# Kernel tuning notes

Hardware: AMD Instinct MI355X
Metric: run time of the kernel (lower is better)

## Reference

```python
import jax, jax.numpy as jnp
import numpy as np

S, D, H, L, FF = 4096, 128, 4, 3, 1024
DH = D // H
LN_EPS = 1e-5


def _layernorm(x, g, b):
    m = jnp.mean(x, axis=-1, keepdims=True)
    v = jnp.mean((x - m) ** 2, axis=-1, keepdims=True)
    return (x - m) * jax.lax.rsqrt(v + LN_EPS) * g + b


def setup_inputs() -> dict:
    key = jax.random.key(0)
    ks = jax.random.split(key, 16)
    w = lambda k, shp, s=0.05: jax.random.normal(k, shp, dtype=jnp.float32) * s
    return {
        "src": jax.random.normal(ks[0], (S, 1, D), dtype=jnp.float32),
        # per-layer transformer params, stacked on leading L axis
        "Wqkv": w(ks[1], (L, 3 * D, D)),
        "bqkv": jnp.zeros((L, 3 * D), jnp.float32),
        "Wo": w(ks[2], (L, D, D)),
        "bo": jnp.zeros((L, D), jnp.float32),
        "ln1_g": jnp.ones((L, D), jnp.float32),
        "ln1_b": jnp.zeros((L, D), jnp.float32),
        "W1": w(ks[3], (L, FF, D)),
        "b1": jnp.zeros((L, FF), jnp.float32),
        "W2": w(ks[4], (L, D, FF)),
        "b2": jnp.zeros((L, D), jnp.float32),
        "ln2_g": jnp.ones((L, D), jnp.float32),
        "ln2_b": jnp.zeros((L, D), jnp.float32),
        "fc1_W": w(ks[5], (D, D)),
        "fc1_b": jnp.zeros((D,), jnp.float32),
        "fc2_W": w(ks[6], (D, D)),
        "fc2_b": jnp.zeros((D,), jnp.float32),
    }


def reference(src, Wqkv, bqkv, Wo, bo, ln1_g, ln1_b, W1, b1, W2, b2,
              ln2_g, ln2_b, fc1_W, fc1_b, fc2_W, fc2_b):
    x = src[:, 0, :]  # [S, D] (batch=1, squeezed as in the torch module)
    scale = 1.0 / np.sqrt(DH).astype(np.float32)
    for l in range(L):  # small fixed layer count
        # --- self-attention (post-norm, as in torch TransformerEncoderLayer, eval mode) ---
        qkv = x @ Wqkv[l].T + bqkv[l]                      # [S, 3D]
        q, k, v = jnp.split(qkv, 3, axis=-1)
        q = q.reshape(S, H, DH)
        k = k.reshape(S, H, DH)
        v = v.reshape(S, H, DH)
        att = jax.nn.softmax(jnp.einsum('shd,thd->hst', q, k) * scale, axis=-1)
        o = jnp.einsum('hst,thd->shd', att, v).reshape(S, D)
        o = o @ Wo[l].T + bo[l]
        x = _layernorm(x + o, ln1_g[l], ln1_b[l])
        # --- feed-forward ---
        f = jax.nn.relu(x @ W1[l].T + b1[l]) @ W2[l].T + b2[l]
        x = _layernorm(x + f, ln2_g[l], ln2_b[l])
    # head
    x = jax.nn.relu(x @ fc1_W.T + fc1_b)
    x = x @ fc2_W.T + fc2_b
    # pairwise cosine similarity, clamped at min 1e-6 (vectorized form of pCosineSim)
    xn = x / jnp.linalg.norm(x, axis=1, keepdims=True)
    return jnp.maximum(xn @ xn.T, 1e-6)
```

## Files before the change

kernel.cpp:

```cpp
#include <hip/hip_runtime.h>
#include <math.h>

#define S 4096
#define QK_SCALE 0.17677669529663687f
#define LOG2E    1.44269504088896f
#define SPLIT 8
#define KS (S / SPLIT)

typedef _Float16 f16x8 __attribute__((ext_vector_type(8)));
typedef _Float16 f16x4 __attribute__((ext_vector_type(4)));
typedef _Float16 f16x2 __attribute__((ext_vector_type(2)));
typedef float f32x4 __attribute__((ext_vector_type(4)));

template<int R>
__device__ __forceinline__ void stageT(_Float16 (*dst)[136], const _Float16* __restrict__ src,
                                       int ld, int row0, int col0, int tid) {
    int r = tid >> 4, cb = (tid & 15) * 8;
#pragma unroll
    for (int v = 0; v < R / 16; v++)
        *(f16x8*)&dst[v * 16 + r][cb] =
            *(const f16x8*)(src + (size_t)(row0 + v * 16 + r) * ld + col0 + cb);
}

__global__ __launch_bounds__(256) void setup_cvt(const float* __restrict__ q,
                                                 const float* __restrict__ wo,
                                                 const float* __restrict__ w1,
                                                 const float* __restrict__ w2,
                                                 const float* __restrict__ f1,
                                                 const float* __restrict__ f2,
                                                 _Float16* __restrict__ dst,
                                                 const float* __restrict__ a,
                                                 float* __restrict__ x,
                                                 _Float16* __restrict__ xh)
{
    int bb = blockIdx.x;
    if (bb < 992) {
        const float* src; size_t dof; int lb;
        if (bb < 144)      { src = q;  dof = 0;      lb = bb; }
        else if (bb < 192) { src = wo; dof = 147456; lb = bb - 144; }
        else if (bb < 576) { src = w1; dof = 196608; lb = bb - 192; }
        else if (bb < 960) { src = w2; dof = 589824; lb = bb - 576; }
        else if (bb < 976) { src = f1; dof = 983040; lb = bb - 960; }
        else               { src = f2; dof = 999424; lb = bb - 976; }
        int i = lb * 1024 + threadIdx.x * 4;
        float4 v = *(const float4*)(src + i);
        f16x4 h = {(_Float16)v.x, (_Float16)v.y, (_Float16)v.z, (_Float16)v.w};
        *(f16x4*)(dst + dof + i) = h;
    } else {
        int i = (bb - 992) * 256 + threadIdx.x;
        float4 v = ((const float4*)a)[i];
        ((float4*)x)[i] = v;
        f16x4 h = {(_Float16)v.x, (_Float16)v.y, (_Float16)v.z, (_Float16)v.w};
        ((f16x4*)xh)[i] = h;
    }
}

__global__ __launch_bounds__(256) void gemm_qkv(const _Float16* __restrict__ xh,
                                                const _Float16* __restrict__ Wh,
                                                const float* __restrict__ bias,
                                                _Float16* __restrict__ qh,
                                                _Float16* __restrict__ kh,
                                                _Float16* __restrict__ vt)
{
    __shared__ _Float16 Ah[16][136], Bh[128][136];
    int tid = threadIdx.x, w = tid >> 6, l = tid & 63, lc = l & 15, lr = l >> 4;
    int m0 = blockIdx.x * 16, by = blockIdx.y;

    stageT<16>(Ah, xh, 128, m0, 0, tid);
    stageT<128>(Bh, Wh, 128, by * 128, 0, tid);
    __syncthreads();

    f32x4 acc[2];
#pragma unroll
    for (int j = 0; j < 2; j++) acc[j] = {0.f, 0.f, 0.f, 0.f};
#pragma unroll
    for (int ks = 0; ks < 4; ks++) {
        f16x8 af = *(const f16x8*)&Ah[lc][ks * 32 + lr * 8];
#pragma unroll
        for (int j = 0; j < 2; j++) {
            f16x8 bf = *(const f16x8*)&Bh[w * 32 + j * 16 + lc][ks * 32 + lr * 8];
            acc[j] = __builtin_amdgcn_mfma_f32_16x16x32_f16(af, bf, acc[j], 0, 0, 0);
        }
    }

    int mb = m0 + lr * 4;
#pragma unroll
    for (int j = 0; j < 2; j++) {
        int n = w * 32 + j * 16 + lc;
        float bb = bias[by * 128 + n];
        if (by == 0) {
#pragma unroll
            for (int r = 0; r < 4; r++)
                qh[(size_t)(mb + r) * 128 + n] =
                    (_Float16)((acc[j][r] + bb) * (QK_SCALE * LOG2E));
        } else if (by == 1) {
            int hh = n >> 5, d = n & 31;
#pragma unroll
            for (int r = 0; r < 4; r++)
                kh[((size_t)hh * S + mb + r) * 32 + d] = (_Float16)(acc[j][r] + bb);
        } else {
            f16x4 pk;
#pragma unroll
            for (int r = 0; r < 4; r++) pk[r] = (_Float16)(acc[j][r] + bb);
            *(f16x4*)&vt[(size_t)n * S + mb] = pk;
        }
    }
}

__global__ __launch_bounds__(256) void attn_mfma(const _Float16* __restrict__ qh,
                                                 const _Float16* __restrict__ kh,
                                                 const _Float16* __restrict__ vt,
                                                 _Float16* __restrict__ part,
                                                 float* __restrict__ mll)
{
    __shared__ _Float16 Ks[2][64][32];
    __shared__ _Float16 Vt[2][32][72];
    __shared__ _Float16 Ps[4][16][72];
    int h = blockIdx.y, q0 = blockIdx.x * 64, z = blockIdx.z;
    int tid = threadIdx.x;
    int w = tid >> 6, l = tid & 63;
    int lc = l & 15, lr = l >> 4;

    f16x8 qf = *(const f16x8*)&qh[(size_t)(q0 + w * 16 + lc) * 128 + h * 32 + lr * 8];

    const _Float16* khh = kh + (size_t)h * S * 32;
    const _Float16* vth = vt + (size_t)h * 32 * S;

    int krow = tid >> 2, kcol = (tid & 3) * 8;
    int vrow = tid >> 3, vcol = (tid & 7) * 8;

    f32x4 o0 = {0.f, 0.f, 0.f, 0.f}, o1 = {0.f, 0.f, 0.f, 0.f};
    float lp = 0.f;

    int k0 = z * KS;
    {
        f16x8 kr = *(const f16x8*)&khh[(size_t)(k0 + krow) * 32 + kcol];
        f16x8 vr = *(const f16x8*)&vth[(size_t)vrow * S + k0 + vcol];
        *(f16x8*)&Ks[0][krow][kcol] = kr;
        *(f16x8*)&Vt[0][vrow][vcol] = vr;
    }
    __syncthreads();

    int cur = 0;
#pragma unroll 1
    for (int t8 = 0; t8 < KS / 64; t8++) {
        bool more = (t8 + 1 < KS / 64);
        f16x8 kr, vr;
        if (more) {
            int kn = k0 + (t8 + 1) * 64;
            kr = *(const f16x8*)&khh[(size_t)(kn + krow) * 32 + kcol];
            vr = *(const f16x8*)&vth[(size_t)vrow * S + kn + vcol];
        }

        f32x4 st[4];
#pragma unroll
        for (int t = 0; t < 4; t++) {
            f16x8 kf = *(const f16x8*)&Ks[cur][t * 16 + lc][lr * 8];
            f32x4 zz = {0.f, 0.f, 0.f, 0.f};
            st[t] = __builtin_amdgcn_mfma_f32_16x16x32_f16(kf, qf, zz, 0, 0, 0);
        }
#pragma unroll
        for (int t = 0; t < 4; t++) {
            float p0 = exp2f(st[t][0]), p1 = exp2f(st[t][1]);
            float p2 = exp2f(st[t][2]), p3 = exp2f(st[t][3]);
            lp += (p0 + p1) + (p2 + p3);
            f16x2 h0 = {(_Float16)p0, (_Float16)p1};
            f16x2 h1 = {(_Float16)p2, (_Float16)p3};
            *(f16x2*)&Ps[w][lc][t * 16 + lr * 4]     = h0;
            *(f16x2*)&Ps[w][lc][t * 16 + lr * 4 + 2] = h1;
        }
        asm volatile("s_waitcnt lgkmcnt(0)" ::: "memory");
#pragma unroll
        for (int ch = 0; ch < 2; ch++) {
            f16x8 pf = *(const f16x8*)&Ps[w][lc][ch * 32 + lr * 8];
            f16x8 v0 = *(const f16x8*)&Vt[cur][lc][ch * 32 + lr * 8];
            f16x8 v1 = *(const f16x8*)&Vt[cur][16 + lc][ch * 32 + lr * 8];
            o0 = __builtin_amdgcn_mfma_f32_16x16x32_f16(pf, v0, o0, 0, 0, 0);
            o1 = __builtin_amdgcn_mfma_f32_16x16x32_f16(pf, v1, o1, 0, 0, 0);
        }
        if (more) {
            *(f16x8*)&Ks[cur ^ 1][krow][kcol] = kr;
            *(f16x8*)&Vt[cur ^ 1][vrow][vcol] = vr;
            __syncthreads();
        }
        cur ^= 1;
    }

    lp += __shfl_xor(lp, 16);
    lp += __shfl_xor(lp, 32);

    _Float16* pz = part + (size_t)z * 524288;
#pragma unroll
    for (int i = 0; i < 4; i++) {
        int q = q0 + w * 16 + lr * 4 + i;
        pz[(size_t)q * 128 + h * 32 + lc]      = (_Float16)o0[i];
        pz[(size_t)q * 128 + h * 32 + 16 + lc] = (_Float16)o1[i];
    }
    if (l < 16) mll[((size_t)z * 4 + h) * 4096 + q0 + w * 16 + lc] = lp;
}

__global__ __launch_bounds__(256) void wo_ln_merge(const _Float16* __restrict__ part,
                                                   const float* __restrict__ mll,
                                                   const _Float16* __restrict__ Wh,
                                                   const float* __restrict__ bias,
                                                   float* __restrict__ x,
                                                   _Float16* __restrict__ xh,
                                                   const float* __restrict__ g,
                                                   const float* __restrict__ b)
{
    __shared__ _Float16 Ah[16][136], Bh[128][136];
    __shared__ float Red[16][4][2];
    int tid = threadIdx.x, w = tid >> 6, l = tid & 63, lc = l & 15, lr = l >> 4;
    int m0 = blockIdx.x * 16;

    {
        int row = tid >> 4, col0 = (tid & 15) * 8;
        int q = m0 + row, hh = col0 >> 5;
        float lsum = 0.f;
#pragma unroll
        for (int s = 0; s < SPLIT; s++) lsum += mll[((size_t)s * 4 + hh) * 4096 + q];
        float am[8];
#pragma unroll
        for (int e = 0; e < 8; e++) am[e] = 0.f;
#pragma unroll
        for (int s = 0; s < SPLIT; s++) {
            f16x8 t = *(const f16x8*)&part[(size_t)s * 524288 + (size_t)q * 128 + col0];
#pragma unroll
            for (int e = 0; e < 8; e++) am[e] += (float)t[e];
        }
        float inv = 1.f / lsum;
        f16x8 hv;
#pragma unroll
        for (int e = 0; e < 8; e++) hv[e] = (_Float16)(am[e] * inv);
        *(f16x8*)&Ah[row][col0] = hv;
    }
    stageT<128>(Bh, Wh, 128, 0, 0, tid);
    __syncthreads();

    f32x4 acc[2];
#pragma unroll
    for (int j = 0; j < 2; j++) acc[j] = {0.f, 0.f, 0.f, 0.f};
#pragma unroll
    for (int ks = 0; ks < 4; ks++) {
        f16x8 af = *(const f16x8*)&Ah[lc][ks * 32 + lr * 8];
#pragma unroll
        for (int j = 0; j < 2; j++) {
            f16x8 bf = *(const f16x8*)&Bh[w * 32 + j * 16 + lc][ks * 32 + lr * 8];
            acc[j] = __builtin_amdgcn_mfma_f32_16x16x32_f16(af, bf, acc[j], 0, 0, 0);
        }
    }

#pragma unroll
    for (int j = 0; j < 2; j++) {
        int n = w * 32 + j * 16 + lc;
        float bb = bias[n];
#pragma unroll
        for (int r = 0; r < 4; r++)
            acc[j][r] += bb + x[(size_t)(m0 + lr * 4 + r) * 128 + n];
    }
#pragma unroll
    for (int r = 0; r < 4; r++) {
        float s1 = acc[0][r] + acc[1][r];
        float s2 = acc[0][r] * acc[0][r] + acc[1][r] * acc[1][r];
#pragma unroll
        for (int off = 1; off < 16; off <<= 1) {
            s1 += __shfl_xor(s1, off);
            s2 += __shfl_xor(s2, off);
        }
        if (lc == 0) { Red[lr * 4 + r][w][0] = s1; Red[lr * 4 + r][w][1] = s2; }
    }
    __syncthreads();
#pragma unroll
    for (int r = 0; r < 4; r++) {
        int rl = lr * 4 + r;
        float S1 = (Red[rl][0][0] + Red[rl][1][0]) + (Red[rl][2][0] + Red[rl][3][0]);
        float S2 = (Red[rl][0][1] + Red[rl][1][1]) + (Red[rl][2][1] + Red[rl][3][1]);
        float mean = S1 * (1.0f / 128.0f);
        float var = S2 * (1.0f / 128.0f) - mean * mean;
        float inv = rsqrtf(var + 1e-5f);
        int m = m0 + rl;
#pragma unroll
        for (int j = 0; j < 2; j++) {
            int n = w * 32 + j * 16 + lc;
            float o = (acc[j][r] - mean) * inv * g[n] + b[n];
            x[(size_t)m * 128 + n] = o;
            xh[(size_t)m * 128 + n] = (_Float16)o;
        }
    }
}

__global__ __launch_bounds__(256) void ffn_pair(const _Float16* __restrict__ xh,
                                                const _Float16* __restrict__ W1h,
                                                const float* __restrict__ b1,
                                                const _Float16* __restrict__ W2h,
                                                _Float16* __restrict__ wpart)
{
    __shared__ _Float16 Ah[64][136], Bh[128][136];
    int tid = threadIdx.x, w = tid >> 6, l = tid & 63, lc = l & 15, lr = l >> 4;
    int wr = w >> 1, wc = w & 1;
    int m0 = blockIdx.x * 64, c = blockIdx.y;

    stageT<64>(Ah, xh, 128, m0, 0, tid);
    stageT<128>(Bh, W1h, 128, c * 128, 0, tid);
    __syncthreads();

    f32x4 acc[2][4];
#pragma unroll
    for (int i = 0; i < 2; i++)
#pragma unroll
        for (int j = 0; j < 4; j++) acc[i][j] = {0.f, 0.f, 0.f, 0.f};
#pragma unroll
    for (int ks = 0; ks < 4; ks++) {
        f16x8 af0 = *(const f16x8*)&Ah[wr * 32 + lc][ks * 32 + lr * 8];
        f16x8 af1 = *(const f16x8*)&Ah[wr * 32 + 16 + lc][ks * 32 + lr * 8];
#pragma unroll
        for (int j = 0; j < 4; j++) {
            f16x8 bf = *(const f16x8*)&Bh[wc * 64 + j * 16 + lc][ks * 32 + lr * 8];
            acc[0][j] = __builtin_amdgcn_mfma_f32_16x16x32_f16(af0, bf, acc[0][j], 0, 0, 0);
            acc[1][j] = __builtin_amdgcn_mfma_f32_16x16x32_f16(af1, bf, acc[1][j], 0, 0, 0);
        }
    }
    __syncthreads();

#pragma unroll
    for (int i = 0; i < 2; i++)
#pragma unroll
        for (int j = 0; j < 4; j++) {
            int n = wc * 64 + j * 16 + lc;
            float bb = b1[c * 128 + n];
#pragma unroll
            for (int r = 0; r < 4; r++)
                Ah[wr * 32 + i * 16 + lr * 4 + r][n] =
                    (_Float16)fmaxf(acc[i][j][r] + bb, 0.f);
        }
    stageT<128>(Bh, W2h, 1024, 0, c * 128, tid);
    __syncthreads();

    f32x4 oacc[2][4];
#pragma unroll
    for (int i = 0; i < 2; i++)
#pragma unroll
        for (int j = 0; j < 4; j++) oacc[i][j] = {0.f, 0.f, 0.f, 0.f};
#pragma unroll
    for (int ks = 0; ks < 4; ks++) {
        f16x8 af0 = *(const f16x8*)&Ah[wr * 32 + lc][ks * 32 + lr * 8];
        f16x8 af1 = *(const f16x8*)&Ah[wr * 32 + 16 + lc][ks * 32 + lr * 8];
#pragma unroll
        for (int j = 0; j < 4; j++) {
            f16x8 bf = *(const f16x8*)&Bh[wc * 64 + j * 16 + lc][ks * 32 + lr * 8];
            oacc[0][j] = __builtin_amdgcn_mfma_f32_16x16x32_f16(af0, bf, oacc[0][j], 0, 0, 0);
            oacc[1][j] = __builtin_amdgcn_mfma_f32_16x16x32_f16(af1, bf, oacc[1][j], 0, 0, 0);
        }
    }

    _Float16* pz = wpart + (size_t)c * 524288;
#pragma unroll
    for (int i = 0; i < 2; i++) {
        int mb = m0 + wr * 32 + i * 16 + lr * 4;
#pragma unroll
        for (int j = 0; j < 4; j++) {
            int n = wc * 64 + j * 16 + lc;
#pragma unroll
            for (int r = 0; r < 4; r++)
                pz[(size_t)(mb + r) * 128 + n] = (_Float16)oacc[i][j][r];
        }
    }
}

__global__ __launch_bounds__(256) void reduce8_ln(const _Float16* __restrict__ part,
                                                  const float* __restrict__ bias,
                                                  float* __restrict__ x,
                                                  _Float16* __restrict__ xh,
                                                  const float* __restrict__ g,
                                                  const float* __restrict__ b)
{
    int row  = blockIdx.x * 4 + (threadIdx.x >> 6);
    int lane = threadIdx.x & 63;
    size_t base = (size_t)row * 128;
    int c = lane * 2;
    float a0 = 0.f, a1 = 0.f;
#pragma unroll
    for (int s = 0; s < 8; s++) {
        f16x2 p = *(const f16x2*)&part[(size_t)s * 524288 + base + c];
        a0 += (float)p[0]; a1 += (float)p[1];
    }
    float2 bv = *(const float2*)&bias[c];
    float2 xv = *(const float2*)&x[base + c];
    a0 += bv.x + xv.x; a1 += bv.y + xv.y;
    float s = a0 + a1;
#pragma unroll
    for (int off = 32; off; off >>= 1) s += __shfl_xor(s, off);
    float mean = s * (1.0f / 128.0f);
    float d0 = a0 - mean, d1 = a1 - mean;
    float v = d0 * d0 + d1 * d1;
#pragma unroll
    for (int off = 32; off; off >>= 1) v += __shfl_xor(v, off);
    float inv = rsqrtf(v * (1.0f / 128.0f) + 1e-5f);
    float2 gv = *(const float2*)&g[c];
    float2 bb = *(const float2*)&b[c];
    float o0 = d0 * inv * gv.x + bb.x, o1 = d1 * inv * gv.y + bb.y;
    float2 r; r.x = o0; r.y = o1;
    *(float2*)&x[base + c] = r;
    f16x2 rh = {(_Float16)o0, (_Float16)o1};
    *(f16x2*)&xh[base + c] = rh;
}

__global__ __launch_bounds__(256) void fc_fused(const _Float16* __restrict__ xh,
                                                const _Float16* __restrict__ W1h,
                                                const float* __restrict__ b1f,
                                                const _Float16* __restrict__ W2h,
                                                const float* __restrict__ b2f,
                                                _Float16* __restrict__ aoh)
{
    __shared__ _Float16 Ah[16][136], Bh[128][136];
    __shared__ float Red[16][4];
    int tid = threadIdx.x, w = tid >> 6, l = tid & 63, lc = l & 15, lr = l >> 4;
    int m0 = blockIdx.x * 16;

    stageT<16>(Ah, xh, 128, m0, 0, tid);
    stageT<128>(Bh, W1h, 128, 0, 0, tid);
    __syncthreads();

    f32x4 acc[2];
#pragma unroll
    for (int j = 0; j < 2; j++) acc[j] = {0.f, 0.f, 0.f, 0.f};
#pragma unroll
    for (int ks = 0; ks < 4; ks++) {
        f16x8 af = *(const f16x8*)&Ah[lc][ks * 32 + lr * 8];
#pragma unroll
        for (int j = 0; j < 2; j++) {
            f16x8 bf = *(const f16x8*)&Bh[w * 32 + j * 16 + lc][ks * 32 + lr * 8];
            acc[j] = __builtin_amdgcn_mfma_f32_16x16x32_f16(af, bf, acc[j], 0, 0, 0);
        }
    }
    __syncthreads();
#pragma unroll
    for (int j = 0; j < 2; j++) {
        int n = w * 32 + j * 16 + lc;
        float bb = b1f[n];
#pragma unroll
        for (int r = 0; r < 4; r++)
            Ah[lr * 4 + r][n] = (_Float16)fmaxf(acc[j][r] + bb, 0.f);
    }
    stageT<128>(Bh, W2h, 128, 0, 0, tid);
    __syncthreads();

    f32x4 o[2];
#pragma unroll
    for (int j = 0; j < 2; j++) o[j] = {0.f, 0.f, 0.f, 0.f};
#pragma unroll
    for (int ks = 0; ks < 4; ks++) {
        f16x8 af = *(const f16x8*)&Ah[lc][ks * 32 + lr * 8];
#pragma unroll
        for (int j = 0; j < 2; j++) {
            f16x8 bf = *(const f16x8*)&Bh[w * 32 + j * 16 + lc][ks * 32 + lr * 8];
            o[j] = __builtin_amdgcn_mfma_f32_16x16x32_f16(af, bf, o[j], 0, 0, 0);
        }
    }
#pragma unroll
    for (int j = 0; j < 2; j++) {
        float bb = b2f[w * 32 + j * 16 + lc];
#pragma unroll
        for (int r = 0; r < 4; r++) o[j][r] += bb;
    }
#pragma unroll
    for (int r = 0; r < 4; r++) {
        float s2 = o[0][r] * o[0][r] + o[1][r] * o[1][r];
#pragma unroll
        for (int off = 1; off < 16; off <<= 1) s2 += __shfl_xor(s2, off);
        if (lc == 0) Red[lr * 4 + r][w] = s2;
    }
    __syncthreads();
#pragma unroll
    for (int r = 0; r < 4; r++) {
        int rl = lr * 4 + r;
        float inv = rsqrtf((Red[rl][0] + Red[rl][1]) + (Red[rl][2] + Red[rl][3]));
        int m = m0 + rl;
#pragma unroll
        for (int j = 0; j < 2; j++) {
            int n = w * 32 + j * 16 + lc;
            aoh[(size_t)m * 128 + n] = (_Float16)(o[j][r] * inv);
        }
    }
}

__global__ __launch_bounds__(256) void gram_f16(const _Float16* __restrict__ aoh,
                                                float* __restrict__ C)
{
    __shared__ _Float16 Ah[64][136], Bh[128][136];
    int tid = threadIdx.x, w = tid >> 6, l = tid & 63, lc = l & 15, lr = l >> 4;
    int wr = w >> 1, wc = w & 1;
    int m0 = blockIdx.x * 64, n0 = blockIdx.y * 128;

    stageT<64>(Ah, aoh, 128, m0, 0, tid);
    stageT<128>(Bh, aoh, 128, n0, 0, tid);
    __syncthreads();

    f32x4 acc[2][4];
#pragma unroll
    for (int i = 0; i < 2; i++)
#pragma unroll
        for (int j = 0; j < 4; j++) acc[i][j] = {0.f, 0.f, 0.f, 0.f};
#pragma unroll
    for (int ks = 0; ks < 4; ks++) {
        f16x8 af0 = *(const f16x8*)&Ah[wr * 32 + lc][ks * 32 + lr * 8];
        f16x8 af1 = *(const f16x8*)&Ah[wr * 32 + 16 + lc][ks * 32 + lr * 8];
#pragma unroll
        for (int j = 0; j < 4; j++) {
            f16x8 bf = *(const f16x8*)&Bh[wc * 64 + j * 16 + lc][ks * 32 + lr * 8];
            acc[0][j] = __builtin_amdgcn_mfma_f32_16x16x32_f16(af0, bf, acc[0][j], 0, 0, 0);
            acc[1][j] = __builtin_amdgcn_mfma_f32_16x16x32_f16(af1, bf, acc[1][j], 0, 0, 0);
        }
    }

#pragma unroll
    for (int i = 0; i < 2; i++) {
        int mb = m0 + wr * 32 + i * 16 + lr * 4;
#pragma unroll
        for (int j = 0; j < 4; j++) {
            int n = n0 + wc * 64 + j * 16 + lc;
#pragma unroll
            for (int r = 0; r < 4; r++)
                C[(size_t)(mb + r) * 4096 + n] = fmaxf(acc[i][j][r], 1e-6f);
        }
    }
}

extern "C" void kernel_launch(void* const* d_in, const int* in_sizes, int n_in,
                              void* d_out, int out_size, void* d_ws, size_t ws_size,
                              hipStream_t stream)
{
    const float* src  = (const float*)d_in[0];
    const float* Wqkv = (const float*)d_in[1];
    const float* bqkv = (const float*)d_in[2];
    const float* Wo   = (const float*)d_in[3];
    const float* bo   = (const float*)d_in[4];
    const float* ln1g = (const float*)d_in[5];
    const float* ln1b = (const float*)d_in[6];
    const float* W1   = (const float*)d_in[7];
    const float* b1   = (const float*)d_in[8];
    const float* W2   = (const float*)d_in[9];
    const float* b2   = (const float*)d_in[10];
    const float* ln2g = (const float*)d_in[11];
    const float* ln2b = (const float*)d_in[12];
    const float* fc1W = (const float*)d_in[13];
    const float* fc1b = (const float*)d_in[14];
    const float* fc2W = (const float*)d_in[15];
    const float* fc2b = (const float*)d_in[16];

    float* ws = (float*)d_ws;
    float*    x   = ws;
    _Float16* xh  = (_Float16*)(ws + 524288);
    _Float16* aoh = (_Float16*)(ws + 786432);
    _Float16* qh  = (_Float16*)(ws + 1048576);
    _Float16* kh  = (_Float16*)(ws + 1310720);
    _Float16* vt  = (_Float16*)(ws + 1572864);
    float*    mll = ws + 1835008;

    _Float16* wpart = (_Float16*)d_out + 4194304;
    _Float16* apart = (_Float16*)d_out + 12582912;
    _Float16* wh    = (_Float16*)d_out + 16777216;
    float*    out   = (float*)d_out;

    _Float16* qkvh = wh;
    _Float16* woh  = wh + 147456;
    _Float16* w1h  = wh + 196608;
    _Float16* w2h  = wh + 589824;
    _Float16* fc1h = wh + 983040;
    _Float16* fc2h = wh + 999424;

    setup_cvt<<<1504, 256, 0, stream>>>(Wqkv, Wo, W1, W2, fc1W, fc2W, wh,
                                        src, x, xh);
    for (int l = 0; l < 3; l++) {
        gemm_qkv<<<dim3(256, 3), 256, 0, stream>>>(xh, qkvh + l * 49152,
                                                   bqkv + l * 384, qh, kh, vt);
        attn_mfma<<<dim3(64, 4, SPLIT), 256, 0, stream>>>(qh, kh, vt, apart, mll);
        wo_ln_merge<<<256, 256, 0, stream>>>(apart, mll, woh + l * 16384, bo + l * 128,
                                             x, xh, ln1g + l * 128, ln1b + l * 128);
        ffn_pair<<<dim3(64, 8), 256, 0, stream>>>(xh, w1h + l * 131072, b1 + l * 1024,
                                                  w2h + l * 131072, wpart);
        reduce8_ln<<<1024, 256, 0, stream>>>(wpart, b2 + l * 128, x, xh,
                                             ln2g + l * 128, ln2b + l * 128);
    }
    fc_fused<<<256, 256, 0, stream>>>(xh, fc1h, fc1b, fc2h, fc2b, aoh);
    gram_f16<<<dim3(64, 32), 256, 0, stream>>>(aoh, out);
}
```

Measured before the change: 263.3 us.

## Stage GEMM tiles via global_load_lds with XOR-swizzled unpadded LDS layout

Replaces the register-staged global-to-LDS copies in all small GEMM kernels with direct global_load_lds transfers of 16 bytes per lane. The padded 136-wide LDS rows become unpadded 128-wide rows with an XOR swizzle on 16-byte groups to avoid bank conflicts, and every fragment read and write goes through the swizzled index. This removes VGPR round-trips and instruction overhead during staging, and in wo_ln_merge lets the weight load overlap the partial-sum merge. The risk is correctness: the direct-to-LDS path needs its wait counts covered by __syncthreads, and the swizzle must match on every write and read.

New measurement: 264.0 us. Within noise of the previous version (+0.3%).

```diff
diff --git a/kernel.cpp b/kernel.cpp
--- a/kernel.cpp
+++ b/kernel.cpp
@@ -12,14 +12,30 @@
 typedef _Float16 f16x2 __attribute__((ext_vector_type(2)));
 typedef float f32x4 __attribute__((ext_vector_type(4)));
 
-template<int R>
-__device__ __forceinline__ void stageT(_Float16 (*dst)[136], const _Float16* __restrict__ src,
-                                       int ld, int row0, int col0, int tid) {
-    int r = tid >> 4, cb = (tid & 15) * 8;
-#pragma unroll
-    for (int v = 0; v < R / 16; v++)
-        *(f16x8*)&dst[v * 16 + r][cb] =
-            *(const f16x8*)(src + (size_t)(row0 + v * 16 + r) * ld + col0 + cb);
+
+template<int ROWS>
+__device__ __forceinline__ void stageGL(_Float16 (*dst)[128], const _Float16* src,
+                                        int ld, int row0, int col0, int tid) {
+    int w = tid >> 6, l = tid & 63;
+    constexpr int NISS = ROWS / 16;
+#pragma unroll
+    for (int v = 0; v < NISS; v++) {
+        int G = (w * NISS + v) * 64 + l;
+        int row = G >> 4, g = G & 15;
+        int gs = g ^ (row & 15);
+        const void* gp = src + (size_t)(row0 + row) * ld + col0 + gs * 8;
+        void* lp = (char*)&dst[0][0] + (size_t)G * 16;
+        __builtin_amdgcn_global_load_lds(
+            (const __attribute__((address_space(1))) void*)gp,
+            (__attribute__((address_space(3))) void*)lp, 16, 0, 0);
+    }
+}
+
+__device__ __forceinline__ f16x8 rdS(const _Float16 (*B)[128], int row, int qg) {
+    return *(const f16x8*)&B[row][(qg ^ (row & 15)) << 3];
+}
+__device__ __forceinline__ void wrS(_Float16 (*B)[128], int row, int col, _Float16 v) {
+    B[row][((((col >> 3) ^ (row & 15))) << 3) | (col & 7)] = v;
 }
 
 __global__ __launch_bounds__(256) void setup_cvt(const float* __restrict__ q,
@@ -62,12 +78,12 @@
                                                 _Float16* __restrict__ kh,
                                                 _Float16* __restrict__ vt)
 {
-    __shared__ _Float16 Ah[16][136], Bh[128][136];
+    __shared__ _Float16 Ah[16][128], Bh[128][128];
     int tid = threadIdx.x, w = tid >> 6, l = tid & 63, lc = l & 15, lr = l >> 4;
     int m0 = blockIdx.x * 16, by = blockIdx.y;
 
-    stageT<16>(Ah, xh, 128, m0, 0, tid);
-    stageT<128>(Bh, Wh, 128, by * 128, 0, tid);
+    stageGL<16>(Ah, xh, 128, m0, 0, tid);
+    stageGL<128>(Bh, Wh, 128, by * 128, 0, tid);
     __syncthreads();
 
     f32x4 acc[2];
@@ -75,10 +91,10 @@
     for (int j = 0; j < 2; j++) acc[j] = {0.f, 0.f, 0.f, 0.f};
 #pragma unroll
     for (int ks = 0; ks < 4; ks++) {
-        f16x8 af = *(const f16x8*)&Ah[lc][ks * 32 + lr * 8];
+        f16x8 af = rdS(Ah, lc, ks * 4 + lr);
 #pragma unroll
         for (int j = 0; j < 2; j++) {
-            f16x8 bf = *(const f16x8*)&Bh[w * 32 + j * 16 + lc][ks * 32 + lr * 8];
+            f16x8 bf = rdS(Bh, w * 32 + j * 16 + lc, ks * 4 + lr);
             acc[j] = __builtin_amdgcn_mfma_f32_16x16x32_f16(af, bf, acc[j], 0, 0, 0);
         }
     }
@@ -208,13 +224,15 @@
                                                    const float* __restrict__ g,
                                                    const float* __restrict__ b)
 {
-    __shared__ _Float16 Ah[16][136], Bh[128][136];
+    __shared__ _Float16 Ah[16][128], Bh[128][128];
     __shared__ float Red[16][4][2];
     int tid = threadIdx.x, w = tid >> 6, l = tid & 63, lc = l & 15, lr = l >> 4;
     int m0 = blockIdx.x * 16;
 
+    stageGL<128>(Bh, Wh, 128, 0, 0, tid);
     {
-        int row = tid >> 4, col0 = (tid & 15) * 8;
+        int row = tid >> 4, qg = tid & 15;
+        int col0 = qg * 8;
         int q = m0 + row, hh = col0 >> 5;
         float lsum = 0.f;
 #pragma unroll
@@ -232,9 +250,8 @@
         f16x8 hv;
 #pragma unroll
         for (int e = 0; e < 8; e++) hv[e] = (_Float16)(am[e] * inv);
-        *(f16x8*)&Ah[row][col0] = hv;
-    }
-    stageT<128>(Bh, Wh, 128, 0, 0, tid);
+        *(f16x8*)&Ah[row][(qg ^ (row & 15)) << 3] = hv;
+    }
     __syncthreads();
 
     f32x4 acc[2];
@@ -242,10 +259,10 @@
     for (int j = 0; j < 2; j++) acc[j] = {0.f, 0.f, 0.f, 0.f};
 #pragma unroll
     for (int ks = 0; ks < 4; ks++) {
-        f16x8 af = *(const f16x8*)&Ah[lc][ks * 32 + lr * 8];
+        f16x8 af = rdS(Ah, lc, ks * 4 + lr);
 #pragma unroll
         for (int j = 0; j < 2; j++) {
-            f16x8 bf = *(const f16x8*)&Bh[w * 32 + j * 16 + lc][ks * 32 + lr * 8];
+            f16x8 bf = rdS(Bh, w * 32 + j * 16 + lc, ks * 4 + lr);
             acc[j] = __builtin_amdgcn_mfma_f32_16x16x32_f16(af, bf, acc[j], 0, 0, 0);
         }
     }
@@ -295,13 +312,13 @@
                                                 const _Float16* __restrict__ W2h,
                                                 _Float16* __restrict__ wpart)
 {
-    __shared__ _Float16 Ah[64][136], Bh[128][136];
+    __shared__ _Float16 Ah[64][128], Bh[128][128];
     int tid = threadIdx.x, w = tid >> 6, l = tid & 63, lc = l & 15, lr = l >> 4;
     int wr = w >> 1, wc = w & 1;
     int m0 = blockIdx.x * 64, c = blockIdx.y;
 
-    stageT<64>(Ah, xh, 128, m0, 0, tid);
-    stageT<128>(Bh, W1h, 128, c * 128, 0, tid);
+    stageGL<64>(Ah, xh, 128, m0, 0, tid);
+    stageGL<128>(Bh, W1h, 128, c * 128, 0, tid);
     __syncthreads();
 
     f32x4 acc[2][4];
@@ -311,11 +328,11 @@
         for (int j = 0; j < 4; j++) acc[i][j] = {0.f, 0.f, 0.f, 0.f};
 #pragma unroll
     for (int ks = 0; ks < 4; ks++) {
-        f16x8 af0 = *(const f16x8*)&Ah[wr * 32 + lc][ks * 32 + lr * 8];
-        f16x8 af1 = *(const f16x8*)&Ah[wr * 32 + 16 + lc][ks * 32 + lr * 8];
+        f16x8 af0 = rdS(Ah, wr * 32 + lc, ks * 4 + lr);
+        f16x8 af1 = rdS(Ah, wr * 32 + 16 + lc, ks * 4 + lr);
 #pragma unroll
         for (int j = 0; j < 4; j++) {
-            f16x8 bf = *(const f16x8*)&Bh[wc * 64 + j * 16 + lc][ks * 32 + lr * 8];
+            f16x8 bf = rdS(Bh, wc * 64 + j * 16 + lc, ks * 4 + lr);
             acc[0][j] = __builtin_amdgcn_mfma_f32_16x16x32_f16(af0, bf, acc[0][j], 0, 0, 0);
             acc[1][j] = __builtin_amdgcn_mfma_f32_16x16x32_f16(af1, bf, acc[1][j], 0, 0, 0);
         }
@@ -330,10 +347,10 @@
             float bb = b1[c * 128 + n];
 #pragma unroll
             for (int r = 0; r < 4; r++)
-                Ah[wr * 32 + i * 16 + lr * 4 + r][n] =
-                    (_Float16)fmaxf(acc[i][j][r] + bb, 0.f);
-        }
-    stageT<128>(Bh, W2h, 1024, 0, c * 128, tid);
+                wrS(Ah, wr * 32 + i * 16 + lr * 4 + r, n,
+                    (_Float16)fmaxf(acc[i][j][r] + bb, 0.f));
+        }
+    stageGL<128>(Bh, W2h, 1024, 0, c * 128, tid);
     __syncthreads();
 
     f32x4 oacc[2][4];
@@ -343,11 +360,11 @@
         for (int j = 0; j < 4; j++) oacc[i][j] = {0.f, 0.f, 0.f, 0.f};
 #pragma unroll
     for (int ks = 0; ks < 4; ks++) {
-        f16x8 af0 = *(const f16x8*)&Ah[wr * 32 + lc][ks * 32 + lr * 8];
-        f16x8 af1 = *(const f16x8*)&Ah[wr * 32 + 16 + lc][ks * 32 + lr * 8];
+        f16x8 af0 = rdS(Ah, wr * 32 + lc, ks * 4 + lr);
+        f16x8 af1 = rdS(Ah, wr * 32 + 16 + lc, ks * 4 + lr);
 #pragma unroll
         for (int j = 0; j < 4; j++) {
-            f16x8 bf = *(const f16x8*)&Bh[wc * 64 + j * 16 + lc][ks * 32 + lr * 8];
+            f16x8 bf = rdS(Bh, wc * 64 + j * 16 + lc, ks * 4 + lr);
             oacc[0][j] = __builtin_amdgcn_mfma_f32_16x16x32_f16(af0, bf, oacc[0][j], 0, 0, 0);
             oacc[1][j] = __builtin_amdgcn_mfma_f32_16x16x32_f16(af1, bf, oacc[1][j], 0, 0, 0);
         }
@@ -412,13 +429,13 @@
                                                 const float* __restrict__ b2f,
                                                 _Float16* __restrict__ aoh)
 {
-    __shared__ _Float16 Ah[16][136], Bh[128][136];
+    __shared__ _Float16 Ah[16][128], Bh[128][128];
     __shared__ float Red[16][4];
     int tid = threadIdx.x, w = tid >> 6, l = tid & 63, lc = l & 15, lr = l >> 4;
     int m0 = blockIdx.x * 16;
 
-    stageT<16>(Ah, xh, 128, m0, 0, tid);
-    stageT<128>(Bh, W1h, 128, 0, 0, tid);
+    stageGL<16>(Ah, xh, 128, m0, 0, tid);
+    stageGL<128>(Bh, W1h, 128, 0, 0, tid);
     __syncthreads();
 
     f32x4 acc[2];
@@ -426,10 +443,10 @@
     for (int j = 0; j < 2; j++) acc[j] = {0.f, 0.f, 0.f, 0.f};
 #pragma unroll
     for (int ks = 0; ks < 4; ks++) {
-        f16x8 af = *(const f16x8*)&Ah[lc][ks * 32 + lr * 8];
+        f16x8 af = rdS(Ah, lc, ks * 4 + lr);
 #pragma unroll
         for (int j = 0; j < 2; j++) {
-            f16x8 bf = *(const f16x8*)&Bh[w * 32 + j * 16 + lc][ks * 32 + lr * 8];
+            f16x8 bf = rdS(Bh, w * 32 + j * 16 + lc, ks * 4 + lr);
             acc[j] = __builtin_amdgcn_mfma_f32_16x16x32_f16(af, bf, acc[j], 0, 0, 0);
         }
     }
@@ -440,9 +457,9 @@
         float bb = b1f[n];
 #pragma unroll
         for (int r = 0; r < 4; r++)
-            Ah[lr * 4 + r][n] = (_Float16)fmaxf(acc[j][r] + bb, 0.f);
-    }
-    stageT<128>(Bh, W2h, 128, 0, 0, tid);
+            wrS(Ah, lr * 4 + r, n, (_Float16)fmaxf(acc[j][r] + bb, 0.f));
+    }
+    stageGL<128>(Bh, W2h, 128, 0, 0, tid);
     __syncthreads();
 
     f32x4 o[2];
@@ -450,10 +467,10 @@
     for (int j = 0; j < 2; j++) o[j] = {0.f, 0.f, 0.f, 0.f};
 #pragma unroll
     for (int ks = 0; ks < 4; ks++) {
-        f16x8 af = *(const f16x8*)&Ah[lc][ks * 32 + lr * 8];
+        f16x8 af = rdS(Ah, lc, ks * 4 + lr);
 #pragma unroll
         for (int j = 0; j < 2; j++) {
-            f16x8 bf = *(const f16x8*)&Bh[w * 32 + j * 16 + lc][ks * 32 + lr * 8];
+            f16x8 bf = rdS(Bh, w * 32 + j * 16 + lc, ks * 4 + lr);
             o[j] = __builtin_amdgcn_mfma_f32_16x16x32_f16(af, bf, o[j], 0, 0, 0);
         }
     }
@@ -487,13 +504,13 @@
 __global__ __launch_bounds__(256) void gram_f16(const _Float16* __restrict__ aoh,
                                                 float* __restrict__ C)
 {
-    __shared__ _Float16 Ah[64][136], Bh[128][136];
+    __shared__ _Float16 Ah[64][128], Bh[128][128];
     int tid = threadIdx.x, w = tid >> 6, l = tid & 63, lc = l & 15, lr = l >> 4;
     int wr = w >> 1, wc = w & 1;
     int m0 = blockIdx.x * 64, n0 = blockIdx.y * 128;
 
-    stageT<64>(Ah, aoh, 128, m0, 0, tid);
-    stageT<128>(Bh, aoh, 128, n0, 0, tid);
+    stageGL<64>(Ah, aoh, 128, m0, 0, tid);
+    stageGL<128>(Bh, aoh, 128, n0, 0, tid);
     __syncthreads();
 
     f32x4 acc[2][4];
@@ -503,11 +520,11 @@
         for (int j = 0; j < 4; j++) acc[i][j] = {0.f, 0.f, 0.f, 0.f};
 #pragma unroll
     for (int ks = 0; ks < 4; ks++) {
-        f16x8 af0 = *(const f16x8*)&Ah[wr * 32 + lc][ks * 32 + lr * 8];
-        f16x8 af1 = *(const f16x8*)&Ah[wr * 32 + 16 + lc][ks * 32 + lr * 8];
+        f16x8 af0 = rdS(Ah, wr * 32 + lc, ks * 4 + lr);
+        f16x8 af1 = rdS(Ah, wr * 32 + 16 + lc, ks * 4 + lr);
 #pragma unroll
         for (int j = 0; j < 4; j++) {
-            f16x8 bf = *(const f16x8*)&Bh[wc * 64 + j * 16 + lc][ks * 32 + lr * 8];
+            f16x8 bf = rdS(Bh, wc * 64 + j * 16 + lc, ks * 4 + lr);
             acc[0][j] = __builtin_amdgcn_mfma_f32_16x16x32_f16(af0, bf, acc[0][j], 0, 0, 0);
             acc[1][j] = __builtin_amdgcn_mfma_f32_16x16x32_f16(af1, bf, acc[1][j], 0, 0, 0);
         }
```
